# Performance work log

Measured on AMD Instinct MI355X. Metric: run time of the kernel, lower is better.

The kernel has to match this reference:

```python
import jax, jax.numpy as jnp
import numpy as np

B, D, H = 4096, 64, 512  # batch, event dim, MLP hidden


def _net(z, t, W1, b1, W2, b2, W3, b3):
    # z: [..., D]; t: scalar, broadcast as a time feature column
    tcol = jnp.broadcast_to(t, z.shape[:-1] + (1,))
    x = jnp.concatenate([z, tcol], axis=-1)            # [..., D+1]
    h = jnp.tanh(x @ W1 + b1)                          # [..., H]
    h = jnp.tanh(h @ W2 + b2)                          # [..., H]
    return h @ W3 + b3                                 # [..., D]


def setup_inputs() -> dict:
    key = jax.random.key(0)
    ks = jax.random.split(key, 6)
    s_in = 1.0 / np.sqrt(D + 1)
    s_h = 1.0 / np.sqrt(H)
    return {
        "z": jax.random.normal(ks[0], (B, D), dtype=jnp.float32),
        "log_pz": jnp.zeros((B, 1), dtype=jnp.float32),
        "t": jax.random.uniform(ks[1], (1,), dtype=jnp.float32),
        "W1": jax.random.normal(ks[2], (D + 1, H), dtype=jnp.float32) * s_in,
        "b1": jnp.zeros((H,), dtype=jnp.float32),
        "W2": jax.random.normal(ks[3], (H, H), dtype=jnp.float32) * s_h,
        "b2": jnp.zeros((H,), dtype=jnp.float32),
        "W3": jax.random.normal(ks[4], (H, D), dtype=jnp.float32) * s_h,
        "b3": jnp.zeros((D,), dtype=jnp.float32),
    }


def reference(z, log_pz, t, W1, b1, W2, b2, W3, b3):
    tval = t[0]
    # velocity field v = net(z, t), batched
    v = _net(z, tval, W1, b1, W2, b2, W3, b3)          # [B, D]
    # exact Jacobian trace: replaces the torch per-dim autograd.grad loop
    # with a fully vectorized per-sample forward-mode Jacobian.
    f_single = lambda zi: _net(zi, tval, W1, b1, W2, b2, W3, b3)  # [D] -> [D]
    jac = jax.vmap(jax.jacfwd(f_single))(z)            # [B, D, D]
    dlogp_dt = -jnp.trace(jac, axis1=1, axis2=2)[:, None]  # [B, 1]
    return (v, dlogp_dt)
```

## Files before the change

kernel.cpp:

```cpp
#include <hip/hip_runtime.h>
#include <hip/hip_bf16.h>

#define BB 4096
#define DD 64
#define HH 512

typedef short short8 __attribute__((ext_vector_type(8)));
typedef float f32x4  __attribute__((ext_vector_type(4)));
typedef __hip_bfloat16 bf16;

__device__ __forceinline__ float tanh_fast(float x) {
    float e = __expf(2.0f * x);
    return 1.0f - __fdividef(2.0f, 1.0f + e);
}

__device__ __forceinline__ void st_swz(bf16* base, int row, int col, int rs, float v) {
    base[row * rs + ((((col >> 3) ^ (row & 7))) << 3) + (col & 7)] = __float2bfloat16(v);
}

__device__ __forceinline__ void st_swz64(bf16* base, int row, int col, int rs,
                                         float a, float b, float c, float d) {
    ushort4 v;
    v.x = __bfloat16_as_ushort(__float2bfloat16(a));
    v.y = __bfloat16_as_ushort(__float2bfloat16(b));
    v.z = __bfloat16_as_ushort(__float2bfloat16(c));
    v.w = __bfloat16_as_ushort(__float2bfloat16(d));
    int e = row * rs + ((((col >> 3) ^ (row & 7))) << 3) + (col & 7);
    *(ushort4*)(base + e) = v;
}

#define GLD1(dst, addr)                                                      \
  asm volatile("global_load_dwordx4 %0, %1, off" : "=&v"(dst) : "v"(addr))

#define GLD2(e0, e1, addr)                                                   \
  asm volatile("global_load_dwordx4 %0, %2, off\n\t"                         \
               "global_load_dwordx4 %1, %2, off offset:1024"                 \
               : "=&v"(e0), "=&v"(e1) : "v"(addr))

#define GLD4(e0, e1, e2, e3, addr)                                           \
  asm volatile("global_load_dwordx4 %0, %4, off\n\t"                         \
               "global_load_dwordx4 %1, %4, off offset:1024\n\t"             \
               "global_load_dwordx4 %2, %4, off offset:2048\n\t"             \
               "global_load_dwordx4 %3, %4, off offset:3072"                 \
               : "=&v"(e0), "=&v"(e1), "=&v"(e2), "=&v"(e3) : "v"(addr))

#define WAITV(n)                                                             \
  do { asm volatile("s_waitcnt vmcnt(" #n ")" ::: "memory");                 \
       __builtin_amdgcn_sched_barrier(0); } while (0)

#define LGKMBAR()                                                            \
  do { asm volatile("s_waitcnt lgkmcnt(0)" ::: "memory");                    \
       __builtin_amdgcn_s_barrier();                                         \
       __builtin_amdgcn_sched_barrier(0); } while (0)

__global__ __launch_bounds__(256) void prep_kernel(
    const float* __restrict__ t, const float* __restrict__ W1,
    const float* __restrict__ b1, const float* __restrict__ W2,
    const float* __restrict__ W3, const float* __restrict__ b3,
    bf16* __restrict__ W1p, bf16* __restrict__ W2p, bf16* __restrict__ W3p,
    bf16* __restrict__ Pp, float* __restrict__ b1eff, float* __restrict__ out)
{
    const int tid  = threadIdx.x;
    const int bx   = blockIdx.x;
    const int lane = tid & 63;
    const int r    = lane & 15;
    const int kq   = lane >> 4;

    if (bx < 160) {
        int T = bx * 4 + (tid >> 6);
        const float* src;
        bf16* dst;
        int stride;
        if (T < 64) {
            int w = T >> 2, s = (T >> 1) & 1, f = T & 1;
            src = W1 + (size_t)(s * 32 + kq * 8) * HH + (w * 2 + f) * 16 + r;
            stride = HH;
            dst = W1p + (size_t)T * 512 + lane * 8;
        } else if (T < 576) {
            int tt = T - 64;
            int cw = tt >> 4, s = tt & 15;
            src = W2 + (size_t)(s * 32 + kq * 8) * HH + cw * 16 + r;
            stride = HH;
            dst = W2p + (size_t)tt * 512 + lane * 8;
        } else {
            int tt = T - 576;
            int q = tt >> 2, f = tt & 3;
            src = W3 + (size_t)(q * 32 + kq * 8) * DD + f * 16 + r;
            stride = DD;
            dst = W3p + (size_t)tt * 512 + lane * 8;
        }
        short8 v;
#pragma unroll
        for (int j = 0; j < 8; ++j)
            v[j] = (short)__bfloat16_as_ushort(__float2bfloat16(src[(size_t)j * stride]));
        *(short8*)dst = v;
    } else if (bx < 672) {
        __shared__ float part[4][64][8];
        int pt = bx - 160;
        int cw = pt >> 4, s = pt & 15;
        int k  = cw * 16 + r;
        int j0 = s * 32 + kq * 8;
        int wq = tid >> 6;
        float acc[8] = {};
        const float* w3row = W3 + (size_t)k * DD + wq * 16;
        const float* w1base = W1 + (size_t)(wq * 16) * HH + j0;
#pragma unroll
        for (int d = 0; d < 16; ++d) {
            float w3 = w3row[d];
            const float4* w1p4 = (const float4*)(w1base + (size_t)d * HH);
            float4 x = w1p4[0], y = w1p4[1];
            acc[0] += x.x * w3; acc[1] += x.y * w3;
            acc[2] += x.z * w3; acc[3] += x.w * w3;
            acc[4] += y.x * w3; acc[5] += y.y * w3;
            acc[6] += y.z * w3; acc[7] += y.w * w3;
        }
        *(f32x4*)&part[wq][lane][0] = *(f32x4*)&acc[0];
        *(f32x4*)&part[wq][lane][4] = *(f32x4*)&acc[4];
        __syncthreads();
        if (wq == 0) {
            short8 v;
#pragma unroll
            for (int j = 0; j < 8; ++j) {
                float ssum = part[0][lane][j] + part[1][lane][j] +
                             part[2][lane][j] + part[3][lane][j];
                v[j] = (short)__bfloat16_as_ushort(
                    __float2bfloat16(ssum * W2[(size_t)(j0 + j) * HH + k]));
            }
            *(short8*)(Pp + (size_t)pt * 512 + lane * 8) = v;
        }
    } else if (bx == 672) {
        float tv = t[0];
        b1eff[tid]       = b1[tid]       + tv * W1[(size_t)64 * HH + tid];
        b1eff[tid + 256] = b1[tid + 256] + tv * W1[(size_t)64 * HH + tid + 256];
    } else {
        int idx = (bx - 673) * 1024 + tid * 4;
        if (idx < BB * DD) {
            int col = idx & 63;
            *(float4*)(out + idx) =
                make_float4(b3[col], b3[col + 1], b3[col + 2], b3[col + 3]);
        } else {
            *(float4*)(out + idx) = make_float4(0.f, 0.f, 0.f, 0.f);
        }
    }
}

__global__ __launch_bounds__(1024, 2) void fused_rows(
    const float* __restrict__ z, const bf16* __restrict__ W1p,
    const bf16* __restrict__ W2p, const bf16* __restrict__ W3p,
    const bf16* __restrict__ Pp, const float* __restrict__ b1eff,
    const float* __restrict__ b2,
    float* __restrict__ outV, float* __restrict__ outTr)
{
    __shared__ alignas(16) char smem[88064];
    bf16* zt   = (bf16*)smem;
    bf16* h1   = (bf16*)(smem + 4096);
    bf16* at   = (bf16*)(smem + 36864);
    bf16* h2   = (bf16*)(smem + 69632);
    float* trp = (float*)(smem + 86016);
    float* vp  = (float*)smem;

    const int tid  = threadIdx.x;
    const int wid  = tid >> 6;
    const int lane = tid & 63;
    const int r    = lane & 15;
    const int kq   = lane >> 4;
    const int rx   = r & 7;
    const int laneE = lane * 8;
    const int rt   = blockIdx.x >> 1;
    const int ch   = blockIdx.x & 1;
    const int bm   = rt * 32;

    float4 b1v0 = *(const float4*)(b1eff + wid * 32 + kq * 4);
    float4 b1v1 = *(const float4*)(b1eff + wid * 32 + 16 + kq * 4);
    float4 b2v  = *(const float4*)(b2 + ch * 256 + wid * 16 + kq * 4);
    asm volatile("" :: "v"(b1v0.x), "v"(b1v0.y), "v"(b1v0.z), "v"(b1v0.w),
                       "v"(b1v1.x), "v"(b1v1.y), "v"(b1v1.z), "v"(b1v1.w),
                       "v"(b2v.x), "v"(b2v.y), "v"(b2v.z), "v"(b2v.w));
    float b1a[2][4] = {{b1v0.x, b1v0.y, b1v0.z, b1v0.w},
                       {b1v1.x, b1v1.y, b1v1.z, b1v1.w}};
    float b2a[4] = {b2v.x, b2v.y, b2v.z, b2v.w};

    {
        int i = tid * 2;
        int row = i >> 6, col = i & 63;
        float2 v = *(const float2*)(z + (size_t)(bm + row) * DD + col);
        st_swz(zt, row, col,     64, v.x);
        st_swz(zt, row, col + 1, 64, v.y);
    }

    short8 q0, q1, q2, q3, p0, p1;
    const bf16* Wb1 = W1p + (size_t)wid * 2048 + laneE;
    GLD2(q0, q1, Wb1);
    GLD2(p0, p1, Wb1 + 1024);
    LGKMBAR();

    f32x4 acc1[2][2] = {};
    WAITV(2);
#pragma unroll
    for (int g = 0; g < 2; ++g) {
        short8 av = *(const short8*)(zt + (g * 16 + r) * 64 + ((kq ^ rx) << 3));
        acc1[g][0] = __builtin_amdgcn_mfma_f32_16x16x32_bf16(q0, av, acc1[g][0], 0, 0, 0);
        acc1[g][1] = __builtin_amdgcn_mfma_f32_16x16x32_bf16(q1, av, acc1[g][1], 0, 0, 0);
    }
    WAITV(0);
#pragma unroll
    for (int g = 0; g < 2; ++g) {
        short8 av = *(const short8*)(zt + (g * 16 + r) * 64 + (((4 + kq) ^ rx) << 3));
        acc1[g][0] = __builtin_amdgcn_mfma_f32_16x16x32_bf16(p0, av, acc1[g][0], 0, 0, 0);
        acc1[g][1] = __builtin_amdgcn_mfma_f32_16x16x32_bf16(p1, av, acc1[g][1], 0, 0, 0);
    }
    short8 rbW[4], rbP[4];
    const bf16* Wb2 = W2p + (size_t)(ch * 16 + wid) * 8192 + laneE;
    const bf16* WbE = Pp  + (size_t)(ch * 16 + wid) * 8192 + laneE;
    GLD1(rbW[0], Wb2);        GLD1(rbP[0], WbE);
    GLD1(rbW[1], Wb2 + 512);  GLD1(rbP[1], WbE + 512);
    GLD1(rbW[2], Wb2 + 1024); GLD1(rbP[2], WbE + 1024);
#pragma unroll
    for (int g = 0; g < 2; ++g)
#pragma unroll
        for (int f = 0; f < 2; ++f) {
            float hv[4], avv[4];
#pragma unroll
            for (int v = 0; v < 4; ++v) {
                hv[v]  = tanh_fast(acc1[g][f][v] + b1a[f][v]);
                avv[v] = fmaf(-hv[v], hv[v], 1.0f);
            }
            int rowq = g * 16 + r;
            int colq = wid * 32 + f * 16 + kq * 4;
            st_swz64(h1, rowq, colq, 512, hv[0], hv[1], hv[2], hv[3]);
            st_swz64(at, rowq, colq, 512, avv[0], avv[1], avv[2], avv[3]);
        }
    LGKMBAR();

    f32x4 acc2[2] = {};
    f32x4 accE[2] = {};
#pragma unroll
    for (int s = 0; s < 16; ++s) {
        int co = (((s * 4 + kq) ^ rx) << 3);
        short8 a1v[2], aav[2];
#pragma unroll
        for (int g = 0; g < 2; ++g) {
            a1v[g] = *(const short8*)(h1 + (g * 16 + r) * 512 + co);
            aav[g] = *(const short8*)(at + (g * 16 + r) * 512 + co);
        }
        if (s + 3 < 16) {
            GLD1(rbW[(s + 3) & 3], Wb2 + (s + 3) * 512);
            GLD1(rbP[(s + 3) & 3], WbE + (s + 3) * 512);
            WAITV(6);
        } else if (s + 2 < 16) { WAITV(4); }
        else if (s + 1 < 16)   { WAITV(2); }
        else                   { WAITV(0); }
#pragma unroll
        for (int g = 0; g < 2; ++g) {
            acc2[g] = __builtin_amdgcn_mfma_f32_16x16x32_bf16(rbW[s & 3], a1v[g], acc2[g], 0, 0, 0);
            accE[g] = __builtin_amdgcn_mfma_f32_16x16x32_bf16(rbP[s & 3], aav[g], accE[g], 0, 0, 0);
        }
    }
    f32x4 bsq[2];
    {
#pragma unroll
        for (int g = 0; g < 2; ++g) {
            float hv[4];
#pragma unroll
            for (int v = 0; v < 4; ++v) {
                hv[v] = tanh_fast(acc2[g][v] + b2a[v]);
                bsq[g][v] = fmaf(-hv[v], hv[v], 1.0f);
            }
            st_swz64(h2, g * 16 + r, wid * 16 + kq * 4, 256,
                     hv[0], hv[1], hv[2], hv[3]);
        }
        const int kw = wid & 7;
        const bf16* Wb3 = W3p + (size_t)(ch * 8 + kw) * 2048 + laneE;
        GLD4(q0, q1, q2, q3, Wb3);
#pragma unroll
        for (int g = 0; g < 2; ++g) {
            float p = accE[g][0] * bsq[g][0] + accE[g][1] * bsq[g][1]
                    + accE[g][2] * bsq[g][2] + accE[g][3] * bsq[g][3];
            p += __shfl_xor(p, 16);
            p += __shfl_xor(p, 32);
            if (lane < 16) trp[wid * 32 + g * 16 + lane] = p;
        }
    }
    LGKMBAR();

    {
        const int kw = wid & 7, rp = wid >> 3;
        f32x4 c0 = {}, c1 = {}, c2 = {}, c3 = {};
        short8 av = *(const short8*)(h2 + (rp * 16 + r) * 256 + (((kw * 4 + kq) ^ rx) << 3));
        WAITV(0);
        c0 = __builtin_amdgcn_mfma_f32_16x16x32_bf16(q0, av, c0, 0, 0, 0);
        c1 = __builtin_amdgcn_mfma_f32_16x16x32_bf16(q1, av, c1, 0, 0, 0);
        c2 = __builtin_amdgcn_mfma_f32_16x16x32_bf16(q2, av, c2, 0, 0, 0);
        c3 = __builtin_amdgcn_mfma_f32_16x16x32_bf16(q3, av, c3, 0, 0, 0);
        int base = kw * 2176 + (rp * 16 + r) * 68 + kq * 4;
        *(f32x4*)(vp + base)      = c0;
        *(f32x4*)(vp + base + 16) = c1;
        *(f32x4*)(vp + base + 32) = c2;
        *(f32x4*)(vp + base + 48) = c3;
    }
    LGKMBAR();

#pragma unroll
    for (int it = 0; it < 2; ++it) {
        int i = it * 1024 + tid;
        int row = i >> 6, col = i & 63;
        float s = 0.f;
#pragma unroll
        for (int kw = 0; kw < 8; ++kw) s += vp[kw * 2176 + row * 68 + col];
        atomicAdd(outV + (size_t)(bm + row) * DD + col, s);
    }
    if (tid < 32) {
        float s = 0.f;
#pragma unroll
        for (int w = 0; w < 16; ++w) s += trp[w * 32 + tid];
        atomicAdd(outTr + bm + tid, -s);
    }
}

extern "C" void kernel_launch(void* const* d_in, const int* in_sizes, int n_in,
                              void* d_out, int out_size, void* d_ws, size_t ws_size,
                              hipStream_t stream)
{
    const float* z  = (const float*)d_in[0];
    const float* t  = (const float*)d_in[2];
    const float* W1 = (const float*)d_in[3];
    const float* b1 = (const float*)d_in[4];
    const float* W2 = (const float*)d_in[5];
    const float* b2 = (const float*)d_in[6];
    const float* W3 = (const float*)d_in[7];
    const float* b3 = (const float*)d_in[8];
    float* out = (float*)d_out;
    float* out_tr = out + (size_t)BB * DD;

    char* w = (char*)d_ws;
    auto alloc = [&](size_t bytes) {
        char* p = w;
        w += (bytes + 255) & ~(size_t)255;
        return p;
    };
    bf16* W1p   = (bf16*)alloc((size_t)64  * 512 * 2);
    bf16* W2p   = (bf16*)alloc((size_t)512 * 512 * 2);
    bf16* W3p   = (bf16*)alloc((size_t)64  * 512 * 2);
    bf16* Pp    = (bf16*)alloc((size_t)512 * 512 * 2);
    float* b1eff = (float*)alloc((size_t)HH * 4);

    prep_kernel<<<933, 256, 0, stream>>>(t, W1, b1, W2, W3, b3,
                                         W1p, W2p, W3p, Pp, b1eff, out);
    fused_rows<<<128 * 2, 1024, 0, stream>>>(z, W1p, W2p, W3p, Pp,
                                             b1eff, b2, out, out_tr);
}
```

Measured before the change: 22.47 us.

## Remap layer-2 warp tiling to 16 rows by 32 cols per warp

Reassigns the second-layer GEMM work so each of the 16 warps handles one 16-row group and two 16-column tiles, instead of all 32 rows and one column tile. Each warp now reads half as much activation data from shared memory but streams twice as much W2/Pp weight data from global memory through a deeper register prefetch ring. The bias, h2 store, trace partial layout and final trace reduction are updated to match the new mapping. This shifts pressure from LDS reads toward global/L2 weight loads and more registers per warp.

```diff
diff --git a/kernel.cpp b/kernel.cpp
--- a/kernel.cpp
+++ b/kernel.cpp
@@ -169,16 +169,21 @@
     const int rt   = blockIdx.x >> 1;
     const int ch   = blockIdx.x & 1;
     const int bm   = rt * 32;
+    const int rg   = wid >> 3;
+    const int cw   = wid & 7;
 
     float4 b1v0 = *(const float4*)(b1eff + wid * 32 + kq * 4);
     float4 b1v1 = *(const float4*)(b1eff + wid * 32 + 16 + kq * 4);
-    float4 b2v  = *(const float4*)(b2 + ch * 256 + wid * 16 + kq * 4);
+    float4 b2v0 = *(const float4*)(b2 + ch * 256 + cw * 32 + kq * 4);
+    float4 b2v1 = *(const float4*)(b2 + ch * 256 + cw * 32 + 16 + kq * 4);
     asm volatile("" :: "v"(b1v0.x), "v"(b1v0.y), "v"(b1v0.z), "v"(b1v0.w),
                        "v"(b1v1.x), "v"(b1v1.y), "v"(b1v1.z), "v"(b1v1.w),
-                       "v"(b2v.x), "v"(b2v.y), "v"(b2v.z), "v"(b2v.w));
+                       "v"(b2v0.x), "v"(b2v0.y), "v"(b2v0.z), "v"(b2v0.w),
+                       "v"(b2v1.x), "v"(b2v1.y), "v"(b2v1.z), "v"(b2v1.w));
     float b1a[2][4] = {{b1v0.x, b1v0.y, b1v0.z, b1v0.w},
                        {b1v1.x, b1v1.y, b1v1.z, b1v1.w}};
-    float b2a[4] = {b2v.x, b2v.y, b2v.z, b2v.w};
+    float b2a[2][4] = {{b2v0.x, b2v0.y, b2v0.z, b2v0.w},
+                       {b2v1.x, b2v1.y, b2v1.z, b2v1.w}};
 
     {
         int i = tid * 2;
@@ -209,12 +214,18 @@
         acc1[g][0] = __builtin_amdgcn_mfma_f32_16x16x32_bf16(p0, av, acc1[g][0], 0, 0, 0);
         acc1[g][1] = __builtin_amdgcn_mfma_f32_16x16x32_bf16(p1, av, acc1[g][1], 0, 0, 0);
     }
-    short8 rbW[4], rbP[4];
-    const bf16* Wb2 = W2p + (size_t)(ch * 16 + wid) * 8192 + laneE;
-    const bf16* WbE = Pp  + (size_t)(ch * 16 + wid) * 8192 + laneE;
-    GLD1(rbW[0], Wb2);        GLD1(rbP[0], WbE);
-    GLD1(rbW[1], Wb2 + 512);  GLD1(rbP[1], WbE + 512);
-    GLD1(rbW[2], Wb2 + 1024); GLD1(rbP[2], WbE + 1024);
+    short8 rW0[4], rW1[4], rP0[4], rP1[4];
+    const bf16* Wb2a = W2p + (size_t)(ch * 16 + cw * 2) * 8192 + laneE;
+    const bf16* Wb2b = Wb2a + 8192;
+    const bf16* WbEa = Pp  + (size_t)(ch * 16 + cw * 2) * 8192 + laneE;
+    const bf16* WbEb = WbEa + 8192;
+#pragma unroll
+    for (int tpre = 0; tpre < 3; ++tpre) {
+        GLD1(rW0[tpre], Wb2a + tpre * 512);
+        GLD1(rW1[tpre], Wb2b + tpre * 512);
+        GLD1(rP0[tpre], WbEa + tpre * 512);
+        GLD1(rP1[tpre], WbEb + tpre * 512);
+    }
 #pragma unroll
     for (int g = 0; g < 2; ++g)
 #pragma unroll
@@ -234,52 +245,49 @@
 
     f32x4 acc2[2] = {};
     f32x4 accE[2] = {};
+    const int arow = rg * 16 + r;
 #pragma unroll
     for (int s = 0; s < 16; ++s) {
         int co = (((s * 4 + kq) ^ rx) << 3);
-        short8 a1v[2], aav[2];
-#pragma unroll
-        for (int g = 0; g < 2; ++g) {
-            a1v[g] = *(const short8*)(h1 + (g * 16 + r) * 512 + co);
-            aav[g] = *(const short8*)(at + (g * 16 + r) * 512 + co);
-        }
+        short8 a1v = *(const short8*)(h1 + arow * 512 + co);
+        short8 aav = *(const short8*)(at + arow * 512 + co);
         if (s + 3 < 16) {
-            GLD1(rbW[(s + 3) & 3], Wb2 + (s + 3) * 512);
-            GLD1(rbP[(s + 3) & 3], WbE + (s + 3) * 512);
-            WAITV(6);
-        } else if (s + 2 < 16) { WAITV(4); }
-        else if (s + 1 < 16)   { WAITV(2); }
+            GLD1(rW0[(s + 3) & 3], Wb2a + (s + 3) * 512);
+            GLD1(rW1[(s + 3) & 3], Wb2b + (s + 3) * 512);
+            GLD1(rP0[(s + 3) & 3], WbEa + (s + 3) * 512);
+            GLD1(rP1[(s + 3) & 3], WbEb + (s + 3) * 512);
+            WAITV(12);
+        } else if (s + 2 < 16) { WAITV(8); }
+        else if (s + 1 < 16)   { WAITV(4); }
         else                   { WAITV(0); }
-#pragma unroll
-        for (int g = 0; g < 2; ++g) {
-            acc2[g] = __builtin_amdgcn_mfma_f32_16x16x32_bf16(rbW[s & 3], a1v[g], acc2[g], 0, 0, 0);
-            accE[g] = __builtin_amdgcn_mfma_f32_16x16x32_bf16(rbP[s & 3], aav[g], accE[g], 0, 0, 0);
-        }
+        acc2[0] = __builtin_amdgcn_mfma_f32_16x16x32_bf16(rW0[s & 3], a1v, acc2[0], 0, 0, 0);
+        acc2[1] = __builtin_amdgcn_mfma_f32_16x16x32_bf16(rW1[s & 3], a1v, acc2[1], 0, 0, 0);
+        accE[0] = __builtin_amdgcn_mfma_f32_16x16x32_bf16(rP0[s & 3], aav, accE[0], 0, 0, 0);
+        accE[1] = __builtin_amdgcn_mfma_f32_16x16x32_bf16(rP1[s & 3], aav, accE[1], 0, 0, 0);
     }
     f32x4 bsq[2];
     {
 #pragma unroll
-        for (int g = 0; g < 2; ++g) {
+        for (int f = 0; f < 2; ++f) {
             float hv[4];
 #pragma unroll
             for (int v = 0; v < 4; ++v) {
-                hv[v] = tanh_fast(acc2[g][v] + b2a[v]);
-                bsq[g][v] = fmaf(-hv[v], hv[v], 1.0f);
+                hv[v] = tanh_fast(acc2[f][v] + b2a[f][v]);
+                bsq[f][v] = fmaf(-hv[v], hv[v], 1.0f);
             }
-            st_swz64(h2, g * 16 + r, wid * 16 + kq * 4, 256,
+            st_swz64(h2, arow, cw * 32 + f * 16 + kq * 4, 256,
                      hv[0], hv[1], hv[2], hv[3]);
         }
         const int kw = wid & 7;
         const bf16* Wb3 = W3p + (size_t)(ch * 8 + kw) * 2048 + laneE;
         GLD4(q0, q1, q2, q3, Wb3);
-#pragma unroll
-        for (int g = 0; g < 2; ++g) {
-            float p = accE[g][0] * bsq[g][0] + accE[g][1] * bsq[g][1]
-                    + accE[g][2] * bsq[g][2] + accE[g][3] * bsq[g][3];
-            p += __shfl_xor(p, 16);
-            p += __shfl_xor(p, 32);
-            if (lane < 16) trp[wid * 32 + g * 16 + lane] = p;
-        }
+        float p = accE[0][0] * bsq[0][0] + accE[0][1] * bsq[0][1]
+                + accE[0][2] * bsq[0][2] + accE[0][3] * bsq[0][3]
+                + accE[1][0] * bsq[1][0] + accE[1][1] * bsq[1][1]
+                + accE[1][2] * bsq[1][2] + accE[1][3] * bsq[1][3];
+        p += __shfl_xor(p, 16);
+        p += __shfl_xor(p, 32);
+        if (lane < 16) trp[wid * 16 + lane] = p;
     }
     LGKMBAR();
 
@@ -310,9 +318,10 @@
         atomicAdd(outV + (size_t)(bm + row) * DD + col, s);
     }
     if (tid < 32) {
+        int rgx = tid >> 4, rl = tid & 15;
         float s = 0.f;
 #pragma unroll
-        for (int w = 0; w < 16; ++w) s += trp[w * 32 + tid];
+        for (int c = 0; c < 8; ++c) s += trp[(rgx * 8 + c) * 16 + rl];
         atomicAdd(outTr + bm + tid, -s);
     }
 }
```

New measurement: 26.43 us. 1.18x slower.

## Retile fused MLP to 64-row blocks with 4-way hidden split and split W2/P streams

Applied to the files above, without the earlier changes.

Each block now handles 64 rows instead of 32 and splits the second-layer hidden dimension four ways instead of two. Half the waves multiply by W2 and the other half by the Jacobian matrix P, each wave covering 32 rows by 32 columns. This doubles reuse of every weight fragment loaded from global memory. The squared-tanh factors go through shared memory so the P waves can form the trace, which adds an extra barrier and raises LDS use to about 154KB. At that size likely only one block fits per CU, lowering occupancy.

```diff
diff --git a/kernel.cpp b/kernel.cpp
--- a/kernel.cpp
+++ b/kernel.cpp
@@ -12,10 +12,6 @@
 __device__ __forceinline__ float tanh_fast(float x) {
     float e = __expf(2.0f * x);
     return 1.0f - __fdividef(2.0f, 1.0f + e);
-}
-
-__device__ __forceinline__ void st_swz(bf16* base, int row, int col, int rs, float v) {
-    base[row * rs + ((((col >> 3) ^ (row & 7))) << 3) + (col & 7)] = __float2bfloat16(v);
 }
 
 __device__ __forceinline__ void st_swz64(bf16* base, int row, int col, int rs,
@@ -151,13 +147,14 @@
     const float* __restrict__ b2,
     float* __restrict__ outV, float* __restrict__ outTr)
 {
-    __shared__ alignas(16) char smem[88064];
+    __shared__ alignas(16) char smem[157696];
     bf16* zt   = (bf16*)smem;
-    bf16* h1   = (bf16*)(smem + 4096);
-    bf16* at   = (bf16*)(smem + 36864);
-    bf16* h2   = (bf16*)(smem + 69632);
-    float* trp = (float*)(smem + 86016);
-    float* vp  = (float*)smem;
+    bf16* h1   = (bf16*)(smem + 8192);
+    bf16* at   = (bf16*)(smem + 73728);
+    float* bsqL = (float*)(smem + 105472);
+    bf16* h2   = (bf16*)(smem + 139264);
+    float* trp = (float*)(smem + 155648);
+    float* vp  = (float*)(smem + 8192);
 
     const int tid  = threadIdx.x;
     const int wid  = tid >> 6;
@@ -166,26 +163,32 @@
     const int kq   = lane >> 4;
     const int rx   = r & 7;
     const int laneE = lane * 8;
-    const int rt   = blockIdx.x >> 1;
-    const int ch   = blockIdx.x & 1;
-    const int bm   = rt * 32;
+    const int rt   = blockIdx.x >> 2;
+    const int ch   = blockIdx.x & 3;
+    const int bm   = rt * 64;
+    const int stream = wid >> 3;
+    const int w8   = wid & 7;
+    const int sw2  = w8 & 3;
+    const int rh   = w8 >> 2;
 
     float4 b1v0 = *(const float4*)(b1eff + wid * 32 + kq * 4);
     float4 b1v1 = *(const float4*)(b1eff + wid * 32 + 16 + kq * 4);
-    float4 b2v  = *(const float4*)(b2 + ch * 256 + wid * 16 + kq * 4);
+    float4 b2v0 = *(const float4*)(b2 + ch * 128 + sw2 * 32 + kq * 4);
+    float4 b2v1 = *(const float4*)(b2 + ch * 128 + sw2 * 32 + 16 + kq * 4);
     asm volatile("" :: "v"(b1v0.x), "v"(b1v0.y), "v"(b1v0.z), "v"(b1v0.w),
                        "v"(b1v1.x), "v"(b1v1.y), "v"(b1v1.z), "v"(b1v1.w),
-                       "v"(b2v.x), "v"(b2v.y), "v"(b2v.z), "v"(b2v.w));
+                       "v"(b2v0.x), "v"(b2v0.y), "v"(b2v0.z), "v"(b2v0.w),
+                       "v"(b2v1.x), "v"(b2v1.y), "v"(b2v1.z), "v"(b2v1.w));
     float b1a[2][4] = {{b1v0.x, b1v0.y, b1v0.z, b1v0.w},
                        {b1v1.x, b1v1.y, b1v1.z, b1v1.w}};
-    float b2a[4] = {b2v.x, b2v.y, b2v.z, b2v.w};
+    float b2a[2][4] = {{b2v0.x, b2v0.y, b2v0.z, b2v0.w},
+                       {b2v1.x, b2v1.y, b2v1.z, b2v1.w}};
 
     {
-        int i = tid * 2;
+        int i = tid * 4;
         int row = i >> 6, col = i & 63;
-        float2 v = *(const float2*)(z + (size_t)(bm + row) * DD + col);
-        st_swz(zt, row, col,     64, v.x);
-        st_swz(zt, row, col + 1, 64, v.y);
+        float4 v = *(const float4*)(z + (size_t)(bm + row) * DD + col);
+        st_swz64(zt, row, col, 64, v.x, v.y, v.z, v.w);
     }
 
     short8 q0, q1, q2, q3, p0, p1;
@@ -194,29 +197,29 @@
     GLD2(p0, p1, Wb1 + 1024);
     LGKMBAR();
 
-    f32x4 acc1[2][2] = {};
+    f32x4 acc1[4][2] = {};
     WAITV(2);
 #pragma unroll
-    for (int g = 0; g < 2; ++g) {
+    for (int g = 0; g < 4; ++g) {
         short8 av = *(const short8*)(zt + (g * 16 + r) * 64 + ((kq ^ rx) << 3));
         acc1[g][0] = __builtin_amdgcn_mfma_f32_16x16x32_bf16(q0, av, acc1[g][0], 0, 0, 0);
         acc1[g][1] = __builtin_amdgcn_mfma_f32_16x16x32_bf16(q1, av, acc1[g][1], 0, 0, 0);
     }
     WAITV(0);
 #pragma unroll
-    for (int g = 0; g < 2; ++g) {
+    for (int g = 0; g < 4; ++g) {
         short8 av = *(const short8*)(zt + (g * 16 + r) * 64 + (((4 + kq) ^ rx) << 3));
         acc1[g][0] = __builtin_amdgcn_mfma_f32_16x16x32_bf16(p0, av, acc1[g][0], 0, 0, 0);
         acc1[g][1] = __builtin_amdgcn_mfma_f32_16x16x32_bf16(p1, av, acc1[g][1], 0, 0, 0);
     }
-    short8 rbW[4], rbP[4];
-    const bf16* Wb2 = W2p + (size_t)(ch * 16 + wid) * 8192 + laneE;
-    const bf16* WbE = Pp  + (size_t)(ch * 16 + wid) * 8192 + laneE;
-    GLD1(rbW[0], Wb2);        GLD1(rbP[0], WbE);
-    GLD1(rbW[1], Wb2 + 512);  GLD1(rbP[1], WbE + 512);
-    GLD1(rbW[2], Wb2 + 1024); GLD1(rbP[2], WbE + 1024);
-#pragma unroll
-    for (int g = 0; g < 2; ++g)
+    short8 rbA[4], rbB[4];
+    const bf16* Wstr = (stream ? Pp : W2p)
+                     + (size_t)(ch * 8 + sw2 * 2) * 8192 + laneE;
+    GLD1(rbA[0], Wstr);        GLD1(rbB[0], Wstr + 8192);
+    GLD1(rbA[1], Wstr + 512);  GLD1(rbB[1], Wstr + 8704);
+    GLD1(rbA[2], Wstr + 1024); GLD1(rbB[2], Wstr + 9216);
+#pragma unroll
+    for (int g = 0; g < 4; ++g)
 #pragma unroll
         for (int f = 0; f < 2; ++f) {
             float hv[4], avv[4];
@@ -232,67 +235,80 @@
         }
     LGKMBAR();
 
-    f32x4 acc2[2] = {};
-    f32x4 accE[2] = {};
+    const bf16* Ab = stream ? at : h1;
+    const int arow0 = rh * 32 + r;
+    f32x4 acc[2][2] = {};
 #pragma unroll
     for (int s = 0; s < 16; ++s) {
         int co = (((s * 4 + kq) ^ rx) << 3);
-        short8 a1v[2], aav[2];
-#pragma unroll
-        for (int g = 0; g < 2; ++g) {
-            a1v[g] = *(const short8*)(h1 + (g * 16 + r) * 512 + co);
-            aav[g] = *(const short8*)(at + (g * 16 + r) * 512 + co);
-        }
+        short8 a0 = *(const short8*)(Ab + arow0 * 512 + co);
+        short8 a1 = *(const short8*)(Ab + (arow0 + 16) * 512 + co);
         if (s + 3 < 16) {
-            GLD1(rbW[(s + 3) & 3], Wb2 + (s + 3) * 512);
-            GLD1(rbP[(s + 3) & 3], WbE + (s + 3) * 512);
+            GLD1(rbA[(s + 3) & 3], Wstr + (s + 3) * 512);
+            GLD1(rbB[(s + 3) & 3], Wstr + 8192 + (s + 3) * 512);
             WAITV(6);
         } else if (s + 2 < 16) { WAITV(4); }
         else if (s + 1 < 16)   { WAITV(2); }
         else                   { WAITV(0); }
+        acc[0][0] = __builtin_amdgcn_mfma_f32_16x16x32_bf16(rbA[s & 3], a0, acc[0][0], 0, 0, 0);
+        acc[0][1] = __builtin_amdgcn_mfma_f32_16x16x32_bf16(rbB[s & 3], a0, acc[0][1], 0, 0, 0);
+        acc[1][0] = __builtin_amdgcn_mfma_f32_16x16x32_bf16(rbA[s & 3], a1, acc[1][0], 0, 0, 0);
+        acc[1][1] = __builtin_amdgcn_mfma_f32_16x16x32_bf16(rbB[s & 3], a1, acc[1][1], 0, 0, 0);
+    }
+    {
+        const int kw = wid & 3;
+        const bf16* Wb3 = W3p + (size_t)(ch * 4 + kw) * 2048 + laneE;
+        GLD4(q0, q1, q2, q3, Wb3);
+    }
+    LGKMBAR();
+
+    if (stream == 0) {
 #pragma unroll
         for (int g = 0; g < 2; ++g) {
-            acc2[g] = __builtin_amdgcn_mfma_f32_16x16x32_bf16(rbW[s & 3], a1v[g], acc2[g], 0, 0, 0);
-            accE[g] = __builtin_amdgcn_mfma_f32_16x16x32_bf16(rbP[s & 3], aav[g], accE[g], 0, 0, 0);
-        }
-    }
-    f32x4 bsq[2];
-    {
+            int rowq = rh * 32 + g * 16 + r;
+#pragma unroll
+            for (int f = 0; f < 2; ++f) {
+                float hv[4];
+                f32x4 bq;
+#pragma unroll
+                for (int v = 0; v < 4; ++v) {
+                    hv[v] = tanh_fast(acc[g][f][v] + b2a[f][v]);
+                    bq[v] = fmaf(-hv[v], hv[v], 1.0f);
+                }
+                int colq = sw2 * 32 + f * 16 + kq * 4;
+                st_swz64(h2, rowq, colq, 128, hv[0], hv[1], hv[2], hv[3]);
+                *(f32x4*)(bsqL + rowq * 132 + colq) = bq;
+            }
+        }
+    }
+    LGKMBAR();
+
+    if (stream == 1) {
 #pragma unroll
         for (int g = 0; g < 2; ++g) {
-            float hv[4];
-#pragma unroll
-            for (int v = 0; v < 4; ++v) {
-                hv[v] = tanh_fast(acc2[g][v] + b2a[v]);
-                bsq[g][v] = fmaf(-hv[v], hv[v], 1.0f);
-            }
-            st_swz64(h2, g * 16 + r, wid * 16 + kq * 4, 256,
-                     hv[0], hv[1], hv[2], hv[3]);
-        }
-        const int kw = wid & 7;
-        const bf16* Wb3 = W3p + (size_t)(ch * 8 + kw) * 2048 + laneE;
-        GLD4(q0, q1, q2, q3, Wb3);
-#pragma unroll
-        for (int g = 0; g < 2; ++g) {
-            float p = accE[g][0] * bsq[g][0] + accE[g][1] * bsq[g][1]
-                    + accE[g][2] * bsq[g][2] + accE[g][3] * bsq[g][3];
+            int rowq = rh * 32 + g * 16 + r;
+            f32x4 bq0 = *(const f32x4*)(bsqL + rowq * 132 + sw2 * 32 + kq * 4);
+            f32x4 bq1 = *(const f32x4*)(bsqL + rowq * 132 + sw2 * 32 + 16 + kq * 4);
+            float p = acc[g][0][0] * bq0[0] + acc[g][0][1] * bq0[1]
+                    + acc[g][0][2] * bq0[2] + acc[g][0][3] * bq0[3]
+                    + acc[g][1][0] * bq1[0] + acc[g][1][1] * bq1[1]
+                    + acc[g][1][2] * bq1[2] + acc[g][1][3] * bq1[3];
             p += __shfl_xor(p, 16);
             p += __shfl_xor(p, 32);
-            if (lane < 16) trp[wid * 32 + g * 16 + lane] = p;
-        }
-    }
-    LGKMBAR();
+            if (lane < 16) trp[sw2 * 64 + rh * 32 + g * 16 + lane] = p;
+        }
+    }
 
     {
-        const int kw = wid & 7, rp = wid >> 3;
+        const int kw = wid & 3, rp = wid >> 2;
         f32x4 c0 = {}, c1 = {}, c2 = {}, c3 = {};
-        short8 av = *(const short8*)(h2 + (rp * 16 + r) * 256 + (((kw * 4 + kq) ^ rx) << 3));
+        short8 av = *(const short8*)(h2 + (rp * 16 + r) * 128 + (((kw * 4 + kq) ^ rx) << 3));
         WAITV(0);
         c0 = __builtin_amdgcn_mfma_f32_16x16x32_bf16(q0, av, c0, 0, 0, 0);
         c1 = __builtin_amdgcn_mfma_f32_16x16x32_bf16(q1, av, c1, 0, 0, 0);
         c2 = __builtin_amdgcn_mfma_f32_16x16x32_bf16(q2, av, c2, 0, 0, 0);
         c3 = __builtin_amdgcn_mfma_f32_16x16x32_bf16(q3, av, c3, 0, 0, 0);
-        int base = kw * 2176 + (rp * 16 + r) * 68 + kq * 4;
+        int base = kw * 4352 + (rp * 16 + r) * 68 + kq * 4;
         *(f32x4*)(vp + base)      = c0;
         *(f32x4*)(vp + base + 16) = c1;
         *(f32x4*)(vp + base + 32) = c2;
@@ -301,18 +317,15 @@
     LGKMBAR();
 
 #pragma unroll
-    for (int it = 0; it < 2; ++it) {
+    for (int it = 0; it < 4; ++it) {
         int i = it * 1024 + tid;
         int row = i >> 6, col = i & 63;
-        float s = 0.f;
-#pragma unroll
-        for (int kw = 0; kw < 8; ++kw) s += vp[kw * 2176 + row * 68 + col];
+        float s = vp[row * 68 + col]        + vp[4352 + row * 68 + col]
+                + vp[8704 + row * 68 + col] + vp[13056 + row * 68 + col];
         atomicAdd(outV + (size_t)(bm + row) * DD + col, s);
     }
-    if (tid < 32) {
-        float s = 0.f;
-#pragma unroll
-        for (int w = 0; w < 16; ++w) s += trp[w * 32 + tid];
+    if (tid < 64) {
+        float s = trp[tid] + trp[64 + tid] + trp[128 + tid] + trp[192 + tid];
         atomicAdd(outTr + bm + tid, -s);
     }
 }
@@ -346,6 +359,6 @@
 
     prep_kernel<<<933, 256, 0, stream>>>(t, W1, b1, W2, W3, b3,
                                          W1p, W2p, W3p, Pp, b1eff, out);
-    fused_rows<<<128 * 2, 1024, 0, stream>>>(z, W1p, W2p, W3p, Pp,
-                                             b1eff, b2, out, out_tr);
-}
+    fused_rows<<<64 * 4, 1024, 0, stream>>>(z, W1p, W2p, W3p, Pp,
+                                            b1eff, b2, out, out_tr);
+}
```

Result: slower. 27.30 us (+21.5%).
